# Kernel optimization log

Measured on AMD Instinct MI355X. Metric: run time of the kernel, lower is better.

Reference implementation:

```python
import jax, jax.numpy as jnp
import numpy as np

# skeletal graph constants
CONN_A = np.array([0,1,2,0,4,5,0,7,8,0,10,11,0,13,14])
CONN_B = np.array([1,2,3,4,5,6,7,8,9,10,11,12,13,14,15])
# angle-limited joints with their (parent, child) from the connection lists
ANG_J = np.array([11,14,5,8]); ANG_P = np.array([10,13,4,7]); ANG_C = np.array([12,15,6,9])


def setup_inputs() -> dict:
    key = jax.random.key(0)
    ks = jax.random.split(key, 16)
    B, T, J, C = 64, 243, 17, 128
    def lin(k, fin, fout):
        kw, kb = jax.random.split(k)
        s = 1.0 / np.sqrt(fin)
        return (jax.random.uniform(kw, (fin, fout), jnp.float32, -s, s),
                jax.random.uniform(kb, (fout,), jnp.float32, -s, s))
    aw1, ab1 = lin(ks[0], C, C // 2)
    aw2, ab2 = lin(ks[1], C // 2, 3)
    bw1, bb1 = lin(ks[2], 2 * C, C)
    bw2, bb2 = lin(ks[3], C, 1)
    cw1, cb1 = lin(ks[4], C * J, 64)
    cw2, cb2 = lin(ks[5], 64, 8)
    return {
        "features": jax.random.normal(ks[6], (B, T, J, C), jnp.float32),
        "pose3d": jax.random.normal(ks[7], (B, T, J, 3), jnp.float32),
        "aw1": aw1, "ab1": ab1, "aw2": aw2, "ab2": ab2,
        "bw1": bw1, "bb1": bb1, "bw2": bw2, "bb2": bb2,
        "cw1": cw1, "cb1": cb1, "cw2": cw2, "cb2": cb2,
    }


def _gelu(x):
    return jax.nn.gelu(x, approximate=False)


def reference(features, pose3d, aw1, ab1, aw2, ab2, bw1, bb1, bw2, bb2, cw1, cb1, cw2, cb2):
    B, T, J, C = features.shape
    # angle predictor: Linear -> GELU -> Linear on every joint feature
    predicted_angles = _gelu(features @ aw1 + ab1) @ aw2 + ab2  # [B,T,J,3]

    # actual bone lengths: vectorized gather over 15 connections
    vec = pose3d[:, :, CONN_B, :] - pose3d[:, :, CONN_A, :]       # [B,T,15,3]
    actual_bone_lengths = jnp.linalg.norm(vec, axis=-1, keepdims=True)  # [B,T,15,1]

    # bone features: concat endpoint features, small MLP
    bone_feat = jnp.concatenate([features[:, :, CONN_A, :], features[:, :, CONN_B, :]], axis=-1)  # [B,T,15,2C]
    predicted_bone_lengths = jax.nn.relu(_gelu(bone_feat @ bw1 + bb1) @ bw2 + bb2)  # [B,T,15,1]

    # actual joint angles at the 4 angle-limited joints, zeros elsewhere
    v1 = pose3d[:, :, ANG_J, :] - pose3d[:, :, ANG_P, :]
    v2 = pose3d[:, :, ANG_C, :] - pose3d[:, :, ANG_J, :]
    v1 = v1 / (jnp.linalg.norm(v1, axis=-1, keepdims=True) + 1e-10)
    v2 = v2 / (jnp.linalg.norm(v2, axis=-1, keepdims=True) + 1e-10)
    dot = jnp.clip(jnp.sum(v1 * v2, axis=-1, keepdims=True), -1 + 1e-7, 1 - 1e-7)
    angle = jnp.arccos(dot)  # [B,T,4,1]
    actual_angles = jnp.zeros((B, T, J, 1), features.dtype).at[:, :, ANG_J, :].set(angle)

    # action classifier on time-averaged flattened joint features
    action_feat = features.reshape(B, T, J * C).mean(axis=1)  # [B,J*C]
    action_logits = _gelu(action_feat @ cw1 + cb1) @ cw2 + cb2  # [B,8]

    return (predicted_angles, actual_angles, predicted_bone_lengths, actual_bone_lengths, action_logits)
```

## Files before the change

kernel.cpp:

```cpp
#include <hip/hip_runtime.h>
#include <math.h>

#define NF 15552
#define NJ 17
#define NC 128
#define JC (NJ*NC)
#define TT 243
#define FB 8

constexpr int cA[15] = {0,1,2,0,4,5,0,7,8,0,10,11,0,13,14};
constexpr int cB[15] = {1,2,3,4,5,6,7,8,9,10,11,12,13,14,15};
constexpr int aJ[4] = {11,14,5,8};
constexpr int aP[4] = {10,13,4,7};
constexpr int aCc[4] = {12,15,6,9};

__device__ const int d_cA16[16] = {0,1,2,0,4,5,0,7,8,0,10,11,0,13,14,0};
__device__ const int d_cB16[16] = {1,2,3,4,5,6,7,8,9,10,11,12,13,14,15,0};

typedef __bf16 bf16x8 __attribute__((ext_vector_type(8)));
typedef float f32x4 __attribute__((ext_vector_type(4)));
typedef unsigned short u16x8 __attribute__((ext_vector_type(8)));

__device__ __forceinline__ float gelu_exact(float x){
  return 0.5f * x * (1.0f + erff(x * 0.7071067811865476f));
}
__device__ __forceinline__ float gelu_fast(float x){
  const float s2 = x * x;
  const float q  = fmaf(s2, -0.1029437f, -2.3021183f);
  const float e  = __builtin_amdgcn_exp2f(q * x);
  return x * __builtin_amdgcn_rcpf(1.0f + e);
}
__device__ __forceinline__ unsigned short bfc(float x){
  return __builtin_bit_cast(unsigned short, (__bf16)x);
}
__device__ __forceinline__ float bf2f(unsigned short u){
  return __builtin_bit_cast(float, ((unsigned)u) << 16);
}

__global__ __launch_bounds__(256) void k_geom(const float* __restrict__ pose,
                                              float* __restrict__ out_aa,
                                              float* __restrict__ out_abl)
{
  const int f = blockIdx.x * 256 + threadIdx.x;
  if (f >= NF) return;
  const float* p = pose + (long)f * NJ * 3;
  float px[NJ], py[NJ], pz[NJ];
  #pragma unroll
  for (int j = 0; j < NJ; ++j){ px[j] = p[3*j]; py[j] = p[3*j+1]; pz[j] = p[3*j+2]; }

  #pragma unroll
  for (int i = 0; i < 15; ++i){
    const int a = cA[i], b = cB[i];
    const float dx = px[b]-px[a], dy = py[b]-py[a], dz = pz[b]-pz[a];
    out_abl[(long)f*15 + i] = sqrtf(dx*dx + dy*dy + dz*dz);
  }

  float ang[NJ];
  #pragma unroll
  for (int j = 0; j < NJ; ++j) ang[j] = 0.0f;
  #pragma unroll
  for (int i = 0; i < 4; ++i){
    const int jj = aJ[i], pp = aP[i], cc = aCc[i];
    float v1x = px[jj]-px[pp], v1y = py[jj]-py[pp], v1z = pz[jj]-pz[pp];
    float v2x = px[cc]-px[jj], v2y = py[cc]-py[jj], v2z = pz[cc]-pz[jj];
    const float n1 = sqrtf(v1x*v1x + v1y*v1y + v1z*v1z) + 1e-10f;
    const float n2 = sqrtf(v2x*v2x + v2y*v2y + v2z*v2z) + 1e-10f;
    v1x /= n1; v1y /= n1; v1z /= n1;
    v2x /= n2; v2y /= n2; v2z /= n2;
    float d = v1x*v2x + v1y*v2y + v1z*v2z;
    d = fminf(fmaxf(d, -1.0f + 1e-7f), 1.0f - 1e-7f);
    ang[jj] = acosf(d);
  }
  #pragma unroll
  for (int j = 0; j < NJ; ++j) out_aa[(long)f*NJ + j] = ang[j];
}

#define SFO(fi, off16) (((fi)*272 + (off16))*8)

__global__ __launch_bounds__(256) void k_fused(const float* __restrict__ feat,
    const float* __restrict__ aw1, const float* __restrict__ ab1,
    const float* __restrict__ aw2, const float* __restrict__ ab2,
    const float* __restrict__ bw1, const float* __restrict__ bb1,
    const float* __restrict__ bw2, const float* __restrict__ bb2,
    float* __restrict__ out_pa, float* __restrict__ out_pbl,
    float* __restrict__ mean_acc)
{
  __shared__ __align__(16) unsigned short s_feat[FB*NJ*NC];
  __shared__ float s_red[4][FB][16];

  const int tid  = threadIdx.x;
  const int w    = tid >> 6;
  const int lane = tid & 63;
  const int g    = lane >> 4;
  const int c    = lane & 15;
  const long f0  = (long)blockIdx.x * FB;

  {
    const float* base = feat + f0 * JC;
    for (int u = tid; u < FB*272; u += 256){
      const float4 v0 = *(const float4*)(base + u*8);
      const float4 v1 = *(const float4*)(base + u*8 + 4);
      u16x8 p;
      p[0]=bfc(v0.x); p[1]=bfc(v0.y); p[2]=bfc(v0.z); p[3]=bfc(v0.w);
      p[4]=bfc(v1.x); p[5]=bfc(v1.y); p[6]=bfc(v1.z); p[7]=bfc(v1.w);
      const int fi = u / 272, r = u - fi*272;
      const int j = r >> 4, kb = r & 15;
      *(u16x8*)&s_feat[SFO(fi, j*16 + (kb ^ (j & 7)))] = p;
    }
  }

  bf16x8 wb[8][2];
  float bb1c[2], bw2c[2];
  #pragma unroll
  for (int nf = 0; nf < 2; ++nf){
    const int col = w*32 + nf*16 + c;
    bb1c[nf] = bb1[col];
    bw2c[nf] = bw2[col];
    #pragma unroll
    for (int ks = 0; ks < 8; ++ks){
      u16x8 t;
      #pragma unroll
      for (int e = 0; e < 8; ++e) t[e] = bfc(bw1[(ks*32 + g*8 + e)*128 + col]);
      wb[ks][nf] = __builtin_bit_cast(bf16x8, t);
    }
  }

  const int jA = d_cA16[c], jB = d_cB16[c];
  int boff[8];
  #pragma unroll
  for (int ks = 0; ks < 8; ++ks){
    const int kk = ks*32 + g*8;
    const int j  = (kk < 128) ? jA : jB;
    const int kb = (kk < 128) ? (ks*4 + g) : (ks*4 + g - 16);
    boff[ks] = j*16 + (kb ^ (j & 7));
  }

  __syncthreads();

  f32x4 bacc[FB][2];
  #pragma unroll
  for (int fi = 0; fi < FB; ++fi){ bacc[fi][0] = (f32x4)0.0f; bacc[fi][1] = (f32x4)0.0f; }

  #pragma unroll
  for (int ks = 0; ks < 8; ++ks){
    bf16x8 av[FB];
    #pragma unroll
    for (int fi = 0; fi < FB; ++fi)
      av[fi] = __builtin_bit_cast(bf16x8, *(const u16x8*)&s_feat[SFO(fi, boff[ks])]);
    #pragma unroll
    for (int fi = 0; fi < FB; ++fi){
      bacc[fi][0] = __builtin_amdgcn_mfma_f32_16x16x32_bf16(av[fi], wb[ks][0], bacc[fi][0], 0, 0, 0);
      bacc[fi][1] = __builtin_amdgcn_mfma_f32_16x16x32_bf16(av[fi], wb[ks][1], bacc[fi][1], 0, 0, 0);
    }
  }

  #pragma unroll
  for (int fi = 0; fi < FB; ++fi){
    float s[4] = {0.f, 0.f, 0.f, 0.f};
    #pragma unroll
    for (int nf = 0; nf < 2; ++nf)
      #pragma unroll
      for (int r = 0; r < 4; ++r)
        s[r] += gelu_fast(bacc[fi][nf][r] + bb1c[nf]) * bw2c[nf];
    #pragma unroll
    for (int r = 0; r < 4; ++r){
      s[r] += __shfl_xor(s[r], 1);
      s[r] += __shfl_xor(s[r], 2);
      s[r] += __shfl_xor(s[r], 4);
      s[r] += __shfl_xor(s[r], 8);
    }
    if (c == 0)
      #pragma unroll
      for (int r = 0; r < 4; ++r) s_red[w][fi][g*4 + r] = s[r];
  }

  bf16x8 wa[4][4];
  float ab1c[4], aw2c[4][3];
  #pragma unroll
  for (int nf = 0; nf < 4; ++nf){
    const int col = nf*16 + c;
    ab1c[nf] = ab1[col];
    #pragma unroll
    for (int m = 0; m < 3; ++m) aw2c[nf][m] = aw2[col*3 + m];
    #pragma unroll
    for (int kt = 0; kt < 4; ++kt){
      u16x8 t;
      #pragma unroll
      for (int e = 0; e < 8; ++e) t[e] = bfc(aw1[(kt*32 + g*8 + e)*64 + col]);
      wa[kt][nf] = __builtin_bit_cast(bf16x8, t);
    }
  }
  const float ab2c[3] = {ab2[0], ab2[1], ab2[2]};

  const int fa0 = 2*w, fa1 = 2*w + 1;
  f32x4 acc0[4], acc1[4], accj[4];
  #pragma unroll
  for (int nf = 0; nf < 4; ++nf){ acc0[nf]=(f32x4)0.0f; acc1[nf]=(f32x4)0.0f; accj[nf]=(f32x4)0.0f; }

  #pragma unroll
  for (int kt = 0; kt < 4; ++kt){
    const int kbx = kt*4 + g;
    const bf16x8 av0 = __builtin_bit_cast(bf16x8,
        *(const u16x8*)&s_feat[SFO(fa0, c*16 + (kbx ^ (c & 7)))]);
    const bf16x8 av1 = __builtin_bit_cast(bf16x8,
        *(const u16x8*)&s_feat[SFO(fa1, c*16 + (kbx ^ (c & 7)))]);
    #pragma unroll
    for (int nf = 0; nf < 4; ++nf){
      acc0[nf] = __builtin_amdgcn_mfma_f32_16x16x32_bf16(av0, wa[kt][nf], acc0[nf], 0, 0, 0);
      acc1[nf] = __builtin_amdgcn_mfma_f32_16x16x32_bf16(av1, wa[kt][nf], acc1[nf], 0, 0, 0);
    }
    if (w == 0){
      const bf16x8 avj = __builtin_bit_cast(bf16x8,
          *(const u16x8*)&s_feat[SFO(c & 7, 16*16 + kbx)]);
      #pragma unroll
      for (int nf = 0; nf < 4; ++nf)
        accj[nf] = __builtin_amdgcn_mfma_f32_16x16x32_bf16(avj, wa[kt][nf], accj[nf], 0, 0, 0);
    }
  }

  #pragma unroll
  for (int half = 0; half < 2; ++half){
    const int fa = half ? fa1 : fa0;
    f32x4* acc = half ? acc1 : acc0;
    float s[4][3];
    #pragma unroll
    for (int r = 0; r < 4; ++r){ s[r][0]=0.f; s[r][1]=0.f; s[r][2]=0.f; }
    #pragma unroll
    for (int nf = 0; nf < 4; ++nf)
      #pragma unroll
      for (int r = 0; r < 4; ++r){
        const float h = gelu_fast(acc[nf][r] + ab1c[nf]);
        s[r][0] = fmaf(h, aw2c[nf][0], s[r][0]);
        s[r][1] = fmaf(h, aw2c[nf][1], s[r][1]);
        s[r][2] = fmaf(h, aw2c[nf][2], s[r][2]);
      }
    #pragma unroll
    for (int r = 0; r < 4; ++r)
      #pragma unroll
      for (int m = 0; m < 3; ++m){
        float v = s[r][m];
        v += __shfl_xor(v, 1);
        v += __shfl_xor(v, 2);
        v += __shfl_xor(v, 4);
        v += __shfl_xor(v, 8);
        s[r][m] = v;
      }
    if (c == 0){
      #pragma unroll
      for (int r = 0; r < 4; ++r){
        const long joint = g*4 + r;
        #pragma unroll
        for (int m = 0; m < 3; ++m)
          out_pa[((f0 + fa)*NJ + joint)*3 + m] = s[r][m] + ab2c[m];
      }
    }
  }
  if (w == 0){
    float s[4][3];
    #pragma unroll
    for (int r = 0; r < 4; ++r){ s[r][0]=0.f; s[r][1]=0.f; s[r][2]=0.f; }
    #pragma unroll
    for (int nf = 0; nf < 4; ++nf)
      #pragma unroll
      for (int r = 0; r < 4; ++r){
        const float h = gelu_fast(accj[nf][r] + ab1c[nf]);
        s[r][0] = fmaf(h, aw2c[nf][0], s[r][0]);
        s[r][1] = fmaf(h, aw2c[nf][1], s[r][1]);
        s[r][2] = fmaf(h, aw2c[nf][2], s[r][2]);
      }
    #pragma unroll
    for (int r = 0; r < 4; ++r)
      #pragma unroll
      for (int m = 0; m < 3; ++m){
        float v = s[r][m];
        v += __shfl_xor(v, 1);
        v += __shfl_xor(v, 2);
        v += __shfl_xor(v, 4);
        v += __shfl_xor(v, 8);
        s[r][m] = v;
      }
    if (c == 0 && g < 2){
      #pragma unroll
      for (int r = 0; r < 4; ++r){
        const long frame = g*4 + r;
        #pragma unroll
        for (int m = 0; m < 3; ++m)
          out_pa[((f0 + frame)*NJ + 16)*3 + m] = s[r][m] + ab2c[m];
      }
    }
  }

  __syncthreads();

  if (tid < FB*15){
    const int fi = tid / 15, row = tid - fi*15;
    const float v = s_red[0][fi][row] + s_red[1][fi][row] +
                    s_red[2][fi][row] + s_red[3][fi][row] + bb2[0];
    out_pbl[(f0 + fi)*15 + row] = fmaxf(v, 0.0f);
  }

  {
    const int b0 = (int)(f0 / TT);
    const int b1 = (int)((f0 + FB - 1) / TT);
    const int split = (b1 > b0) ? (b1*TT - (int)f0) : FB;
    for (int jc = tid; jc < JC; jc += 256){
      const int j = jc >> 7, k = jc & 127;
      const int eoff = (j*16 + ((k >> 3) ^ (j & 7)))*8 + (k & 7);
      float s0 = 0.f, s1 = 0.f;
      #pragma unroll
      for (int fi = 0; fi < FB; ++fi){
        const float v = bf2f(s_feat[fi*JC + eoff]);
        if (fi < split) s0 += v; else s1 += v;
      }
      atomicAdd(&mean_acc[(long)b0*JC + jc], s0);
      if (b1 > b0) atomicAdd(&mean_acc[(long)b1*JC + jc], s1);
    }
  }
}

__global__ __launch_bounds__(256) void k_action(const float* __restrict__ sum_src,
    const float* __restrict__ cw1, const float* __restrict__ cb1,
    const float* __restrict__ cw2, const float* __restrict__ cb2,
    float* __restrict__ out_lg)
{
  __shared__ float s_m[JC];
  __shared__ float s_part[4][64];
  __shared__ float s_h[64];
  const int b = blockIdx.x, tid = threadIdx.x;
  for (int i = tid; i < JC; i += 256) s_m[i] = sum_src[(long)b*JC + i] * (1.0f/243.0f);
  __syncthreads();
  const int n = tid & 63, part = tid >> 6;
  float s = 0.0f;
  const int k0 = part * 544;
  for (int k = k0; k < k0 + 544; ++k) s = fmaf(s_m[k], cw1[(long)k*64 + n], s);
  s_part[part][n] = s;
  __syncthreads();
  if (tid < 64) s_h[tid] = gelu_exact(s_part[0][tid] + s_part[1][tid] +
                                      s_part[2][tid] + s_part[3][tid] + cb1[tid]);
  __syncthreads();
  if (tid < 8){
    float v = cb2[tid];
    #pragma unroll
    for (int k = 0; k < 64; ++k) v = fmaf(s_h[k], cw2[k*8 + tid], v);
    out_lg[b*8 + tid] = v;
  }
}

extern "C" void kernel_launch(void* const* d_in, const int* in_sizes, int n_in,
                              void* d_out, int out_size, void* d_ws, size_t ws_size,
                              hipStream_t stream)
{
  const float* feat = (const float*)d_in[0];
  const float* pose = (const float*)d_in[1];
  const float* aw1  = (const float*)d_in[2];
  const float* ab1  = (const float*)d_in[3];
  const float* aw2  = (const float*)d_in[4];
  const float* ab2  = (const float*)d_in[5];
  const float* bw1  = (const float*)d_in[6];
  const float* bb1  = (const float*)d_in[7];
  const float* bw2  = (const float*)d_in[8];
  const float* bb2  = (const float*)d_in[9];
  const float* cw1  = (const float*)d_in[10];
  const float* cb1  = (const float*)d_in[11];
  const float* cw2  = (const float*)d_in[12];
  const float* cb2  = (const float*)d_in[13];

  float* out = (float*)d_out;
  float* out_pa  = out;
  float* out_aa  = out + 793152;
  float* out_pbl = out + 1057536;
  float* out_abl = out + 1290816;
  float* out_lg  = out + 1524096;

  float* mean_acc = (float*)d_ws;
  hipMemsetAsync(mean_acc, 0, (size_t)64 * JC * sizeof(float), stream);

  k_geom<<<dim3((NF + 255)/256), dim3(256), 0, stream>>>(pose, out_aa, out_abl);
  k_fused<<<dim3(NF/FB), dim3(256), 0, stream>>>(feat, aw1, ab1, aw2, ab2,
                                                 bw1, bb1, bw2, bb2,
                                                 out_pa, out_pbl, mean_acc);
  k_action<<<dim3(64), dim3(256), 0, stream>>>(mean_acc, cw1, cb1, cw2, cb2, out_lg);
}
```

Baseline: 146.9 us.

## Make fused kernel persistent with double-buffered LDS staging and register-held mean sums

The fused kernel now runs each block over 16 iterations of 4 frames (243 blocks instead of 1944). It double-buffers the bf16 feature tile in LDS so the next tile's global loads overlap compute on the current one. Weights are loaded into registers once per block. Time-mean partial sums stay in registers and are flushed with atomics once per block, which cuts atomic traffic. The memset is folded into k_geom, removing one launch. The cost is fewer blocks (one per CU at most, via launch_bounds) and a serialized per-iteration loop, which may leave memory latency exposed.

```diff
diff --git a/kernel.cpp b/kernel.cpp
--- a/kernel.cpp
+++ b/kernel.cpp
@@ -6,7 +6,9 @@
 #define NC 128
 #define JC (NJ*NC)
 #define TT 243
-#define FB 8
+#define FB 4
+#define NIT 16
+#define FRB (FB*NIT)
 
 constexpr int cA[15] = {0,1,2,0,4,5,0,7,8,0,10,11,0,13,14};
 constexpr int cB[15] = {1,2,3,4,5,6,7,8,9,10,11,12,13,14,15};
@@ -39,8 +41,12 @@
 
 __global__ __launch_bounds__(256) void k_geom(const float* __restrict__ pose,
                                               float* __restrict__ out_aa,
-                                              float* __restrict__ out_abl)
+                                              float* __restrict__ out_abl,
+                                              float* __restrict__ mean_acc)
 {
+  for (long i = (long)blockIdx.x*256 + threadIdx.x; i < 64L*JC; i += (long)gridDim.x*256)
+    mean_acc[i] = 0.0f;
+
   const int f = blockIdx.x * 256 + threadIdx.x;
   if (f >= NF) return;
   const float* p = pose + (long)f * NJ * 3;
@@ -77,7 +83,7 @@
 
 #define SFO(fi, off16) (((fi)*272 + (off16))*8)
 
-__global__ __launch_bounds__(256) void k_fused(const float* __restrict__ feat,
+__global__ __launch_bounds__(256, 1) void k_fused(const float* __restrict__ feat,
     const float* __restrict__ aw1, const float* __restrict__ ab1,
     const float* __restrict__ aw2, const float* __restrict__ ab2,
     const float* __restrict__ bw1, const float* __restrict__ bb1,
@@ -85,7 +91,7 @@
     float* __restrict__ out_pa, float* __restrict__ out_pbl,
     float* __restrict__ mean_acc)
 {
-  __shared__ __align__(16) unsigned short s_feat[FB*NJ*NC];
+  __shared__ __align__(16) unsigned short s_feat[2][FB*NJ*NC];
   __shared__ float s_red[4][FB][16];
 
   const int tid  = threadIdx.x;
@@ -93,21 +99,28 @@
   const int lane = tid & 63;
   const int g    = lane >> 4;
   const int c    = lane & 15;
-  const long f0  = (long)blockIdx.x * FB;
-
-  {
-    const float* base = feat + f0 * JC;
-    for (int u = tid; u < FB*272; u += 256){
-      const float4 v0 = *(const float4*)(base + u*8);
-      const float4 v1 = *(const float4*)(base + u*8 + 4);
-      u16x8 p;
-      p[0]=bfc(v0.x); p[1]=bfc(v0.y); p[2]=bfc(v0.z); p[3]=bfc(v0.w);
-      p[4]=bfc(v1.x); p[5]=bfc(v1.y); p[6]=bfc(v1.z); p[7]=bfc(v1.w);
-      const int fi = u / 272, r = u - fi*272;
-      const int j = r >> 4, kb = r & 15;
-      *(u16x8*)&s_feat[SFO(fi, j*16 + (kb ^ (j & 7)))] = p;
-    }
-  }
+  const long F0  = (long)blockIdx.x * FRB;
+
+  auto stage = [&](int bsel, int it){
+    const float* base = feat + (F0 + (long)it*FB) * JC;
+    unsigned short* dst = s_feat[bsel];
+    #pragma unroll
+    for (int u0 = 0; u0 < FB*272; u0 += 256){
+      const int u = u0 + tid;
+      if (u < FB*272){
+        const float4 v0 = *(const float4*)(base + u*8);
+        const float4 v1 = *(const float4*)(base + u*8 + 4);
+        u16x8 p;
+        p[0]=bfc(v0.x); p[1]=bfc(v0.y); p[2]=bfc(v0.z); p[3]=bfc(v0.w);
+        p[4]=bfc(v1.x); p[5]=bfc(v1.y); p[6]=bfc(v1.z); p[7]=bfc(v1.w);
+        const int fi = u / 272, r = u - fi*272;
+        const int j = r >> 4, kb = r & 15;
+        *(u16x8*)&dst[SFO(fi, j*16 + (kb ^ (j & 7)))] = p;
+      }
+    }
+  };
+
+  stage(0, 0);
 
   bf16x8 wb[8][2];
   float bb1c[2], bw2c[2];
@@ -124,6 +137,24 @@
       wb[ks][nf] = __builtin_bit_cast(bf16x8, t);
     }
   }
+  bf16x8 wa[4][4];
+  float ab1c[4], aw2c[4][3];
+  #pragma unroll
+  for (int nf = 0; nf < 4; ++nf){
+    const int col = nf*16 + c;
+    ab1c[nf] = ab1[col];
+    #pragma unroll
+    for (int m = 0; m < 3; ++m) aw2c[nf][m] = aw2[col*3 + m];
+    #pragma unroll
+    for (int kt = 0; kt < 4; ++kt){
+      u16x8 t;
+      #pragma unroll
+      for (int e = 0; e < 8; ++e) t[e] = bfc(aw1[(kt*32 + g*8 + e)*64 + col]);
+      wa[kt][nf] = __builtin_bit_cast(bf16x8, t);
+    }
+  }
+  const float ab2c[3] = {ab2[0], ab2[1], ab2[2]};
+  const float bb2c = bb2[0];
 
   const int jA = d_cA16[c], jB = d_cB16[c];
   int boff[8];
@@ -135,185 +166,173 @@
     boff[ks] = j*16 + (kb ^ (j & 7));
   }
 
-  __syncthreads();
-
-  f32x4 bacc[FB][2];
-  #pragma unroll
-  for (int fi = 0; fi < FB; ++fi){ bacc[fi][0] = (f32x4)0.0f; bacc[fi][1] = (f32x4)0.0f; }
-
-  #pragma unroll
-  for (int ks = 0; ks < 8; ++ks){
-    bf16x8 av[FB];
-    #pragma unroll
-    for (int fi = 0; fi < FB; ++fi)
-      av[fi] = __builtin_bit_cast(bf16x8, *(const u16x8*)&s_feat[SFO(fi, boff[ks])]);
+  const int b0    = (int)(F0 / TT);
+  const int split = min(FRB, TT - (int)(F0 - (long)b0*TT));
+  float m0[9], m1[9];
+  #pragma unroll
+  for (int s = 0; s < 9; ++s){ m0[s] = 0.f; m1[s] = 0.f; }
+
+  int buf = 0;
+  for (int it = 0; it < NIT; ++it){
+    __syncthreads();
+    if (it + 1 < NIT) stage(buf ^ 1, it + 1);
+
+    const unsigned short* fb = s_feat[buf];
+
+    f32x4 bacc[FB][2];
+    #pragma unroll
+    for (int fi = 0; fi < FB; ++fi){ bacc[fi][0] = (f32x4)0.0f; bacc[fi][1] = (f32x4)0.0f; }
+    #pragma unroll
+    for (int ks = 0; ks < 8; ++ks){
+      bf16x8 av[FB];
+      #pragma unroll
+      for (int fi = 0; fi < FB; ++fi)
+        av[fi] = __builtin_bit_cast(bf16x8, *(const u16x8*)&fb[SFO(fi, boff[ks])]);
+      #pragma unroll
+      for (int fi = 0; fi < FB; ++fi){
+        bacc[fi][0] = __builtin_amdgcn_mfma_f32_16x16x32_bf16(av[fi], wb[ks][0], bacc[fi][0], 0, 0, 0);
+        bacc[fi][1] = __builtin_amdgcn_mfma_f32_16x16x32_bf16(av[fi], wb[ks][1], bacc[fi][1], 0, 0, 0);
+      }
+    }
     #pragma unroll
     for (int fi = 0; fi < FB; ++fi){
-      bacc[fi][0] = __builtin_amdgcn_mfma_f32_16x16x32_bf16(av[fi], wb[ks][0], bacc[fi][0], 0, 0, 0);
-      bacc[fi][1] = __builtin_amdgcn_mfma_f32_16x16x32_bf16(av[fi], wb[ks][1], bacc[fi][1], 0, 0, 0);
-    }
-  }
-
-  #pragma unroll
-  for (int fi = 0; fi < FB; ++fi){
-    float s[4] = {0.f, 0.f, 0.f, 0.f};
-    #pragma unroll
-    for (int nf = 0; nf < 2; ++nf)
+      float s[4] = {0.f, 0.f, 0.f, 0.f};
+      #pragma unroll
+      for (int nf = 0; nf < 2; ++nf)
+        #pragma unroll
+        for (int r = 0; r < 4; ++r)
+          s[r] += gelu_fast(bacc[fi][nf][r] + bb1c[nf]) * bw2c[nf];
+      #pragma unroll
+      for (int r = 0; r < 4; ++r){
+        s[r] += __shfl_xor(s[r], 1);
+        s[r] += __shfl_xor(s[r], 2);
+        s[r] += __shfl_xor(s[r], 4);
+        s[r] += __shfl_xor(s[r], 8);
+      }
+      if (c == 0)
+        #pragma unroll
+        for (int r = 0; r < 4; ++r) s_red[w][fi][g*4 + r] = s[r];
+    }
+
+    f32x4 acc0[4], accj[4];
+    #pragma unroll
+    for (int nf = 0; nf < 4; ++nf){ acc0[nf]=(f32x4)0.0f; accj[nf]=(f32x4)0.0f; }
+    #pragma unroll
+    for (int kt = 0; kt < 4; ++kt){
+      const int kbx = kt*4 + g;
+      const bf16x8 av0 = __builtin_bit_cast(bf16x8,
+          *(const u16x8*)&fb[SFO(w, c*16 + (kbx ^ (c & 7)))]);
+      #pragma unroll
+      for (int nf = 0; nf < 4; ++nf)
+        acc0[nf] = __builtin_amdgcn_mfma_f32_16x16x32_bf16(av0, wa[kt][nf], acc0[nf], 0, 0, 0);
+      if (w == 0){
+        const bf16x8 avj = __builtin_bit_cast(bf16x8,
+            *(const u16x8*)&fb[SFO(c & 3, 16*16 + kbx)]);
+        #pragma unroll
+        for (int nf = 0; nf < 4; ++nf)
+          accj[nf] = __builtin_amdgcn_mfma_f32_16x16x32_bf16(avj, wa[kt][nf], accj[nf], 0, 0, 0);
+      }
+    }
+    {
+      float s[4][3];
+      #pragma unroll
+      for (int r = 0; r < 4; ++r){ s[r][0]=0.f; s[r][1]=0.f; s[r][2]=0.f; }
+      #pragma unroll
+      for (int nf = 0; nf < 4; ++nf)
+        #pragma unroll
+        for (int r = 0; r < 4; ++r){
+          const float h = gelu_fast(acc0[nf][r] + ab1c[nf]);
+          s[r][0] = fmaf(h, aw2c[nf][0], s[r][0]);
+          s[r][1] = fmaf(h, aw2c[nf][1], s[r][1]);
+          s[r][2] = fmaf(h, aw2c[nf][2], s[r][2]);
+        }
       #pragma unroll
       for (int r = 0; r < 4; ++r)
-        s[r] += gelu_fast(bacc[fi][nf][r] + bb1c[nf]) * bw2c[nf];
-    #pragma unroll
-    for (int r = 0; r < 4; ++r){
-      s[r] += __shfl_xor(s[r], 1);
-      s[r] += __shfl_xor(s[r], 2);
-      s[r] += __shfl_xor(s[r], 4);
-      s[r] += __shfl_xor(s[r], 8);
-    }
-    if (c == 0)
-      #pragma unroll
-      for (int r = 0; r < 4; ++r) s_red[w][fi][g*4 + r] = s[r];
-  }
-
-  bf16x8 wa[4][4];
-  float ab1c[4], aw2c[4][3];
-  #pragma unroll
-  for (int nf = 0; nf < 4; ++nf){
-    const int col = nf*16 + c;
-    ab1c[nf] = ab1[col];
-    #pragma unroll
-    for (int m = 0; m < 3; ++m) aw2c[nf][m] = aw2[col*3 + m];
-    #pragma unroll
-    for (int kt = 0; kt < 4; ++kt){
-      u16x8 t;
-      #pragma unroll
-      for (int e = 0; e < 8; ++e) t[e] = bfc(aw1[(kt*32 + g*8 + e)*64 + col]);
-      wa[kt][nf] = __builtin_bit_cast(bf16x8, t);
-    }
-  }
-  const float ab2c[3] = {ab2[0], ab2[1], ab2[2]};
-
-  const int fa0 = 2*w, fa1 = 2*w + 1;
-  f32x4 acc0[4], acc1[4], accj[4];
-  #pragma unroll
-  for (int nf = 0; nf < 4; ++nf){ acc0[nf]=(f32x4)0.0f; acc1[nf]=(f32x4)0.0f; accj[nf]=(f32x4)0.0f; }
-
-  #pragma unroll
-  for (int kt = 0; kt < 4; ++kt){
-    const int kbx = kt*4 + g;
-    const bf16x8 av0 = __builtin_bit_cast(bf16x8,
-        *(const u16x8*)&s_feat[SFO(fa0, c*16 + (kbx ^ (c & 7)))]);
-    const bf16x8 av1 = __builtin_bit_cast(bf16x8,
-        *(const u16x8*)&s_feat[SFO(fa1, c*16 + (kbx ^ (c & 7)))]);
-    #pragma unroll
-    for (int nf = 0; nf < 4; ++nf){
-      acc0[nf] = __builtin_amdgcn_mfma_f32_16x16x32_bf16(av0, wa[kt][nf], acc0[nf], 0, 0, 0);
-      acc1[nf] = __builtin_amdgcn_mfma_f32_16x16x32_bf16(av1, wa[kt][nf], acc1[nf], 0, 0, 0);
+        #pragma unroll
+        for (int m = 0; m < 3; ++m){
+          float v = s[r][m];
+          v += __shfl_xor(v, 1);
+          v += __shfl_xor(v, 2);
+          v += __shfl_xor(v, 4);
+          v += __shfl_xor(v, 8);
+          s[r][m] = v;
+        }
+      if (c == 0){
+        const long frame = F0 + (long)it*FB + w;
+        #pragma unroll
+        for (int r = 0; r < 4; ++r){
+          const int joint = g*4 + r;
+          #pragma unroll
+          for (int m = 0; m < 3; ++m)
+            out_pa[(frame*NJ + joint)*3 + m] = s[r][m] + ab2c[m];
+        }
+      }
     }
     if (w == 0){
-      const bf16x8 avj = __builtin_bit_cast(bf16x8,
-          *(const u16x8*)&s_feat[SFO(c & 7, 16*16 + kbx)]);
+      float s[4][3];
+      #pragma unroll
+      for (int r = 0; r < 4; ++r){ s[r][0]=0.f; s[r][1]=0.f; s[r][2]=0.f; }
       #pragma unroll
       for (int nf = 0; nf < 4; ++nf)
-        accj[nf] = __builtin_amdgcn_mfma_f32_16x16x32_bf16(avj, wa[kt][nf], accj[nf], 0, 0, 0);
-    }
-  }
-
-  #pragma unroll
-  for (int half = 0; half < 2; ++half){
-    const int fa = half ? fa1 : fa0;
-    f32x4* acc = half ? acc1 : acc0;
-    float s[4][3];
-    #pragma unroll
-    for (int r = 0; r < 4; ++r){ s[r][0]=0.f; s[r][1]=0.f; s[r][2]=0.f; }
-    #pragma unroll
-    for (int nf = 0; nf < 4; ++nf)
-      #pragma unroll
-      for (int r = 0; r < 4; ++r){
-        const float h = gelu_fast(acc[nf][r] + ab1c[nf]);
-        s[r][0] = fmaf(h, aw2c[nf][0], s[r][0]);
-        s[r][1] = fmaf(h, aw2c[nf][1], s[r][1]);
-        s[r][2] = fmaf(h, aw2c[nf][2], s[r][2]);
-      }
-    #pragma unroll
-    for (int r = 0; r < 4; ++r)
-      #pragma unroll
-      for (int m = 0; m < 3; ++m){
-        float v = s[r][m];
-        v += __shfl_xor(v, 1);
-        v += __shfl_xor(v, 2);
-        v += __shfl_xor(v, 4);
-        v += __shfl_xor(v, 8);
-        s[r][m] = v;
-      }
-    if (c == 0){
-      #pragma unroll
-      for (int r = 0; r < 4; ++r){
-        const long joint = g*4 + r;
-        #pragma unroll
-        for (int m = 0; m < 3; ++m)
-          out_pa[((f0 + fa)*NJ + joint)*3 + m] = s[r][m] + ab2c[m];
-      }
-    }
-  }
-  if (w == 0){
-    float s[4][3];
-    #pragma unroll
-    for (int r = 0; r < 4; ++r){ s[r][0]=0.f; s[r][1]=0.f; s[r][2]=0.f; }
-    #pragma unroll
-    for (int nf = 0; nf < 4; ++nf)
-      #pragma unroll
-      for (int r = 0; r < 4; ++r){
-        const float h = gelu_fast(accj[nf][r] + ab1c[nf]);
-        s[r][0] = fmaf(h, aw2c[nf][0], s[r][0]);
-        s[r][1] = fmaf(h, aw2c[nf][1], s[r][1]);
-        s[r][2] = fmaf(h, aw2c[nf][2], s[r][2]);
-      }
-    #pragma unroll
-    for (int r = 0; r < 4; ++r)
-      #pragma unroll
-      for (int m = 0; m < 3; ++m){
-        float v = s[r][m];
-        v += __shfl_xor(v, 1);
-        v += __shfl_xor(v, 2);
-        v += __shfl_xor(v, 4);
-        v += __shfl_xor(v, 8);
-        s[r][m] = v;
-      }
-    if (c == 0 && g < 2){
-      #pragma unroll
-      for (int r = 0; r < 4; ++r){
-        const long frame = g*4 + r;
-        #pragma unroll
-        for (int m = 0; m < 3; ++m)
-          out_pa[((f0 + frame)*NJ + 16)*3 + m] = s[r][m] + ab2c[m];
-      }
-    }
-  }
-
-  __syncthreads();
-
-  if (tid < FB*15){
-    const int fi = tid / 15, row = tid - fi*15;
-    const float v = s_red[0][fi][row] + s_red[1][fi][row] +
-                    s_red[2][fi][row] + s_red[3][fi][row] + bb2[0];
-    out_pbl[(f0 + fi)*15 + row] = fmaxf(v, 0.0f);
-  }
-
-  {
-    const int b0 = (int)(f0 / TT);
-    const int b1 = (int)((f0 + FB - 1) / TT);
-    const int split = (b1 > b0) ? (b1*TT - (int)f0) : FB;
-    for (int jc = tid; jc < JC; jc += 256){
-      const int j = jc >> 7, k = jc & 127;
-      const int eoff = (j*16 + ((k >> 3) ^ (j & 7)))*8 + (k & 7);
-      float s0 = 0.f, s1 = 0.f;
-      #pragma unroll
-      for (int fi = 0; fi < FB; ++fi){
-        const float v = bf2f(s_feat[fi*JC + eoff]);
-        if (fi < split) s0 += v; else s1 += v;
-      }
-      atomicAdd(&mean_acc[(long)b0*JC + jc], s0);
-      if (b1 > b0) atomicAdd(&mean_acc[(long)b1*JC + jc], s1);
+        #pragma unroll
+        for (int r = 0; r < 4; ++r){
+          const float h = gelu_fast(accj[nf][r] + ab1c[nf]);
+          s[r][0] = fmaf(h, aw2c[nf][0], s[r][0]);
+          s[r][1] = fmaf(h, aw2c[nf][1], s[r][1]);
+          s[r][2] = fmaf(h, aw2c[nf][2], s[r][2]);
+        }
+      #pragma unroll
+      for (int r = 0; r < 4; ++r)
+        #pragma unroll
+        for (int m = 0; m < 3; ++m){
+          float v = s[r][m];
+          v += __shfl_xor(v, 1);
+          v += __shfl_xor(v, 2);
+          v += __shfl_xor(v, 4);
+          v += __shfl_xor(v, 8);
+          s[r][m] = v;
+        }
+      if (c == 0 && g == 0){
+        #pragma unroll
+        for (int r = 0; r < 4; ++r){
+          const long frame = F0 + (long)it*FB + r;
+          #pragma unroll
+          for (int m = 0; m < 3; ++m)
+            out_pa[(frame*NJ + 16)*3 + m] = s[r][m] + ab2c[m];
+        }
+      }
+    }
+
+    #pragma unroll
+    for (int s = 0; s < 9; ++s){
+      const int jc = tid + s*256;
+      if (jc < JC){
+        const int j = jc >> 7, k = jc & 127;
+        const int eoff = (j*16 + ((k >> 3) ^ (j & 7)))*8 + (k & 7);
+        #pragma unroll
+        for (int fi = 0; fi < FB; ++fi){
+          const float v = bf2f(fb[fi*JC + eoff]);
+          if (it*FB + fi < split) m0[s] += v; else m1[s] += v;
+        }
+      }
+    }
+
+    __syncthreads();
+    if (tid < FB*15){
+      const int fi = tid / 15, row = tid - fi*15;
+      const float v = s_red[0][fi][row] + s_red[1][fi][row] +
+                      s_red[2][fi][row] + s_red[3][fi][row] + bb2c;
+      out_pbl[(F0 + (long)it*FB + fi)*15 + row] = fmaxf(v, 0.0f);
+    }
+    buf ^= 1;
+  }
+
+  #pragma unroll
+  for (int s = 0; s < 9; ++s){
+    const int jc = tid + s*256;
+    if (jc < JC){
+      atomicAdd(&mean_acc[(long)b0*JC + jc], m0[s]);
+      if (split < FRB) atomicAdd(&mean_acc[(long)(b0+1)*JC + jc], m1[s]);
     }
   }
 }
@@ -373,11 +392,10 @@
   float* out_lg  = out + 1524096;
 
   float* mean_acc = (float*)d_ws;
-  hipMemsetAsync(mean_acc, 0, (size_t)64 * JC * sizeof(float), stream);
-
-  k_geom<<<dim3((NF + 255)/256), dim3(256), 0, stream>>>(pose, out_aa, out_abl);
-  k_fused<<<dim3(NF/FB), dim3(256), 0, stream>>>(feat, aw1, ab1, aw2, ab2,
-                                                 bw1, bb1, bw2, bb2,
-                                                 out_pa, out_pbl, mean_acc);
+
+  k_geom<<<dim3((NF + 255)/256), dim3(256), 0, stream>>>(pose, out_aa, out_abl, mean_acc);
+  k_fused<<<dim3(NF/FRB), dim3(256), 0, stream>>>(feat, aw1, ab1, aw2, ab2,
+                                                  bw1, bb1, bw2, bb2,
+                                                  out_pa, out_pbl, mean_acc);
   k_action<<<dim3(64), dim3(256), 0, stream>>>(mean_acc, cw1, cb1, cw2, cb2, out_lg);
 }
```

New measurement: 145.1 us. About the same (-1.2%).
